# Kernel tuning notes

Measured on AMD Instinct MI355X. Metric: run time of the kernel, lower is better.

The kernel has to match this reference:

```python
import jax, jax.numpy as jnp
import numpy as np

NUM_HEADS = 32
HEAD_DIM = 128
HEAVY_BUDGET = 256
RECENT_BUDGET = 256
ROPE_BASE = 10000.0


def _rope_tables(position_ids, head_dim, dtype):
    inv_freq = 1.0 / (ROPE_BASE ** (jnp.arange(0, head_dim, 2, dtype=jnp.float32) / head_dim))
    freqs = position_ids.astype(jnp.float32)[..., None] * inv_freq  # [b, s, hd/2]
    emb = jnp.concatenate([freqs, freqs], axis=-1)                  # [b, s, hd]
    return jnp.cos(emb).astype(dtype), jnp.sin(emb).astype(dtype)


def _rotate_half(x):
    h = x.shape[-1] // 2
    return jnp.concatenate([-x[..., h:], x[..., :h]], axis=-1)


def setup_inputs() -> dict:
    key = jax.random.key(0)
    k1, k2, k3, k4, k5 = jax.random.split(key, 5)
    b, s, d = 1, 2048, 4096
    hidden_states = jax.random.normal(k1, (b, s, d), dtype=jnp.float32)
    # additive causal mask, as HF passes into forward
    neg = jnp.finfo(jnp.float32).min
    causal = jnp.tril(jnp.ones((s, s), dtype=bool))
    attention_mask = jnp.where(causal, 0.0, neg).astype(jnp.float32)[None, None]  # [1,1,s,s]
    position_ids = jnp.arange(s, dtype=jnp.int32)[None]  # [1, s]
    scale = 0.02
    Wq = jax.random.normal(k2, (d, d), dtype=jnp.float32) * scale
    Wk = jax.random.normal(k3, (d, d), dtype=jnp.float32) * scale
    Wv = jax.random.normal(k4, (d, d), dtype=jnp.float32) * scale
    Wo = jax.random.normal(k5, (d, d), dtype=jnp.float32) * scale
    return {"hidden_states": hidden_states, "attention_mask": attention_mask,
            "position_ids": position_ids, "Wq": Wq, "Wk": Wk, "Wv": Wv, "Wo": Wo}


def reference(hidden_states, attention_mask, position_ids, Wq, Wk, Wv, Wo):
    b, s, d = hidden_states.shape
    H, hd = NUM_HEADS, HEAD_DIM
    kv = s  # prefill: no past_key_value, masks reset

    # projections: nn.Linear(x) = x @ W.T
    q = (hidden_states @ Wq.T).reshape(b, s, H, hd).transpose(0, 2, 1, 3)  # [b,H,s,hd]
    k = (hidden_states @ Wk.T).reshape(b, s, H, hd).transpose(0, 2, 1, 3)
    v = (hidden_states @ Wv.T).reshape(b, s, H, hd).transpose(0, 2, 1, 3)

    cos, sin = _rope_tables(position_ids, hd, q.dtype)  # [b,s,hd]
    cos, sin = cos[:, None], sin[:, None]               # broadcast over heads
    q = q * cos + _rotate_half(q) * sin
    k = k * cos + _rotate_half(k) * sin

    attn = jnp.einsum('bhqd,bhkd->bhqk', q, k) / np.float32(np.sqrt(hd))
    neg = jnp.finfo(attn.dtype).min
    attn = jnp.maximum(attn + attention_mask, neg)
    # attention_masks_next is None on the first (prefill) call -> no multiplicative mask here
    attn = jax.nn.softmax(attn.astype(jnp.float32), axis=-1).astype(q.dtype)  # [b,H,s,kv]

    # running per-head score accumulation: sum over batch and query dims
    scores = attn.sum(axis=0).sum(axis=1)  # [H, kv]; previous_scores is None at prefill

    # heavy-hitter eviction mask for the next decode step (kv+1 columns)
    mask = jnp.ones((H, kv + 1), dtype=attn.dtype)
    # attn_tokens_all (=kv) > cache_budget, recent_budget > 0:
    mask = mask.at[:, :kv + 1 - RECENT_BUDGET].set(0.0)
    selected = scores[:, :kv - RECENT_BUDGET]                    # drop recent region
    _, keep_topk = jax.lax.top_k(selected, HEAVY_BUDGET)         # [H, heavy]
    mask = mask.at[jnp.arange(H)[:, None], keep_topk].set(1.0)   # scatter heavy hitters
    # torch aliasing: score_mask = attn_mask[:, :-1]; score_mask[:, -recent:] = 1 mutates attn_mask too
    mask = mask.at[:, kv - RECENT_BUDGET:kv].set(1.0)
    attention_masks_next = mask[None, :, None, :]                # [1,H,1,kv+1]
    previous_scores = scores * mask[:, :kv]                      # masked score state

    out = jnp.einsum('bhqk,bhkd->bhqd', attn, v)                 # [b,H,s,hd]
    out = out.transpose(0, 2, 1, 3).reshape(b, s, d) @ Wo.T
    return out, attention_masks_next, previous_scores
```

## Files before the change

### kernel.cpp

```cpp
#include <hip/hip_runtime.h>
#include <hip/hip_bf16.h>
#include <cmath>

#define S_LEN 2048
#define DMODEL 4096
#define NH 32
#define HDIM 128
#define HEAVY 256
#define RECENT 256
#define ATTN_SCALE 0.08838834764831845f
#define NEGBIG -3.0e38f
#define MB (1024ull * 1024ull)

typedef __attribute__((ext_vector_type(8))) short short8v;
typedef __attribute__((ext_vector_type(4))) short short4v;
typedef __attribute__((ext_vector_type(4))) float floatx4;

__device__ inline ushort f2bf(float x) {
  __hip_bfloat16 h = __float2bfloat16(x);
  return __builtin_bit_cast(ushort, h);
}
__device__ inline float bf2f(ushort u) {
  __hip_bfloat16 h = __builtin_bit_cast(__hip_bfloat16, u);
  return __bfloat162float(h);
}
struct Split3 {
  short a, b, c;
};
__device__ inline Split3 split3(float x) {
  Split3 o;
  ushort u1 = f2bf(x);
  float r1 = x - bf2f(u1);
  ushort u2 = f2bf(r1);
  float r2 = r1 - bf2f(u2);
  ushort u3 = f2bf(r2);
  o.a = (short)u1;
  o.b = (short)u2;
  o.c = (short)u3;
  return o;
}

__global__ __launch_bounds__(256) void gemm6(const float* __restrict__ A,
                                             const float* __restrict__ B,
                                             float* __restrict__ C, int M, int N, int K) {
  __shared__ short Aa[128 * 40], Ab[128 * 40], Ac[128 * 40];
  __shared__ short Ba[128 * 40], Bb[128 * 40], Bc[128 * 40];
  const int tid = threadIdx.x;
  const int w = tid >> 6, l = tid & 63, g = l >> 4, ln = l & 15;
  const int wm = w >> 1, wn = w & 1;
  const int row0 = blockIdx.y * 128, col0 = blockIdx.x * 128;
  floatx4 acc[4][4] = {};
  for (int k0 = 0; k0 < K; k0 += 32) {
    __syncthreads();
#pragma unroll
    for (int i = 0; i < 4; i++) {
      int id = tid + i * 256;
      int r = id >> 3, c4 = id & 7;
      float4 av = *reinterpret_cast<const float4*>(&A[(size_t)(row0 + r) * K + k0 + c4 * 4]);
      float4 bv = *reinterpret_cast<const float4*>(&B[(size_t)(col0 + r) * K + k0 + c4 * 4]);
      float af[4] = {av.x, av.y, av.z, av.w};
      float bf[4] = {bv.x, bv.y, bv.z, bv.w};
      short4v a1, a2, a3, b1, b2, b3;
#pragma unroll
      for (int j = 0; j < 4; j++) {
        Split3 sa = split3(af[j]);
        Split3 sb = split3(bf[j]);
        a1[j] = sa.a; a2[j] = sa.b; a3[j] = sa.c;
        b1[j] = sb.a; b2[j] = sb.b; b3[j] = sb.c;
      }
      int o = r * 40 + c4 * 4;
      *reinterpret_cast<short4v*>(&Aa[o]) = a1;
      *reinterpret_cast<short4v*>(&Ab[o]) = a2;
      *reinterpret_cast<short4v*>(&Ac[o]) = a3;
      *reinterpret_cast<short4v*>(&Ba[o]) = b1;
      *reinterpret_cast<short4v*>(&Bb[o]) = b2;
      *reinterpret_cast<short4v*>(&Bc[o]) = b3;
    }
    __syncthreads();
#pragma unroll
    for (int i = 0; i < 4; i++) {
      int ar = (wm * 64 + i * 16 + ln) * 40 + g * 8;
      short8v a1 = *reinterpret_cast<const short8v*>(&Aa[ar]);
      short8v a2 = *reinterpret_cast<const short8v*>(&Ab[ar]);
      short8v a3 = *reinterpret_cast<const short8v*>(&Ac[ar]);
#pragma unroll
      for (int j = 0; j < 4; j++) {
        int br = (wn * 64 + j * 16 + ln) * 40 + g * 8;
        short8v b1 = *reinterpret_cast<const short8v*>(&Ba[br]);
        short8v b2 = *reinterpret_cast<const short8v*>(&Bb[br]);
        short8v b3 = *reinterpret_cast<const short8v*>(&Bc[br]);
        acc[i][j] = __builtin_amdgcn_mfma_f32_16x16x32_bf16(a1, b1, acc[i][j], 0, 0, 0);
        acc[i][j] = __builtin_amdgcn_mfma_f32_16x16x32_bf16(a1, b2, acc[i][j], 0, 0, 0);
        acc[i][j] = __builtin_amdgcn_mfma_f32_16x16x32_bf16(a2, b1, acc[i][j], 0, 0, 0);
        acc[i][j] = __builtin_amdgcn_mfma_f32_16x16x32_bf16(a1, b3, acc[i][j], 0, 0, 0);
        acc[i][j] = __builtin_amdgcn_mfma_f32_16x16x32_bf16(a2, b2, acc[i][j], 0, 0, 0);
        acc[i][j] = __builtin_amdgcn_mfma_f32_16x16x32_bf16(a3, b1, acc[i][j], 0, 0, 0);
      }
    }
  }
#pragma unroll
  for (int i = 0; i < 4; i++)
#pragma unroll
    for (int j = 0; j < 4; j++)
#pragma unroll
      for (int r = 0; r < 4; r++)
        C[(size_t)(row0 + wm * 64 + i * 16 + g * 4 + r) * N + col0 + wn * 64 + j * 16 + ln] =
            acc[i][j][r];
}

__global__ __launch_bounds__(256) void gemm_bf1(const float* __restrict__ A,
                                                const float* __restrict__ B,
                                                float* __restrict__ C, int M, int N, int K) {
  __shared__ short Ah[128 * 40];
  __shared__ short Bh[128 * 40];
  const int tid = threadIdx.x;
  const int w = tid >> 6, l = tid & 63, g = l >> 4, ln = l & 15;
  const int wm = w >> 1, wn = w & 1;
  const int row0 = blockIdx.y * 128, col0 = blockIdx.x * 128;
  floatx4 acc[4][4] = {};
  for (int k0 = 0; k0 < K; k0 += 32) {
    __syncthreads();
#pragma unroll
    for (int i = 0; i < 4; i++) {
      int id = tid + i * 256;
      int r = id >> 3, c4 = id & 7;
      float4 av = *reinterpret_cast<const float4*>(&A[(size_t)(row0 + r) * K + k0 + c4 * 4]);
      float4 bv = *reinterpret_cast<const float4*>(&B[(size_t)(col0 + r) * K + k0 + c4 * 4]);
      short4v ah, bh;
      ah[0] = (short)f2bf(av.x); ah[1] = (short)f2bf(av.y);
      ah[2] = (short)f2bf(av.z); ah[3] = (short)f2bf(av.w);
      bh[0] = (short)f2bf(bv.x); bh[1] = (short)f2bf(bv.y);
      bh[2] = (short)f2bf(bv.z); bh[3] = (short)f2bf(bv.w);
      *reinterpret_cast<short4v*>(&Ah[r * 40 + c4 * 4]) = ah;
      *reinterpret_cast<short4v*>(&Bh[r * 40 + c4 * 4]) = bh;
    }
    __syncthreads();
#pragma unroll
    for (int i = 0; i < 4; i++) {
      short8v a = *reinterpret_cast<const short8v*>(&Ah[(wm * 64 + i * 16 + ln) * 40 + g * 8]);
#pragma unroll
      for (int j = 0; j < 4; j++) {
        short8v b = *reinterpret_cast<const short8v*>(&Bh[(wn * 64 + j * 16 + ln) * 40 + g * 8]);
        acc[i][j] = __builtin_amdgcn_mfma_f32_16x16x32_bf16(a, b, acc[i][j], 0, 0, 0);
      }
    }
  }
#pragma unroll
  for (int i = 0; i < 4; i++)
#pragma unroll
    for (int j = 0; j < 4; j++)
#pragma unroll
      for (int r = 0; r < 4; r++)
        C[(size_t)(row0 + wm * 64 + i * 16 + g * 4 + r) * N + col0 + wn * 64 + j * 16 + ln] =
            acc[i][j][r];
}

__global__ __launch_bounds__(256) void gemm_vbt(const float* __restrict__ A,
                                                const float* __restrict__ B,
                                                ushort* __restrict__ Vt, int M, int N, int K) {
  __shared__ short Ah[128 * 40];
  __shared__ short Bh[128 * 40];
  const int tid = threadIdx.x;
  const int w = tid >> 6, l = tid & 63, g = l >> 4, ln = l & 15;
  const int wm = w >> 1, wn = w & 1;
  const int row0 = blockIdx.y * 128, col0 = blockIdx.x * 128;
  floatx4 acc[4][4] = {};
  for (int k0 = 0; k0 < K; k0 += 32) {
    __syncthreads();
#pragma unroll
    for (int i = 0; i < 4; i++) {
      int id = tid + i * 256;
      int r = id >> 3, c4 = id & 7;
      float4 av = *reinterpret_cast<const float4*>(&A[(size_t)(row0 + r) * K + k0 + c4 * 4]);
      float4 bv = *reinterpret_cast<const float4*>(&B[(size_t)(col0 + r) * K + k0 + c4 * 4]);
      short4v ah, bh;
      ah[0] = (short)f2bf(av.x); ah[1] = (short)f2bf(av.y);
      ah[2] = (short)f2bf(av.z); ah[3] = (short)f2bf(av.w);
      bh[0] = (short)f2bf(bv.x); bh[1] = (short)f2bf(bv.y);
      bh[2] = (short)f2bf(bv.z); bh[3] = (short)f2bf(bv.w);
      *reinterpret_cast<short4v*>(&Ah[r * 40 + c4 * 4]) = ah;
      *reinterpret_cast<short4v*>(&Bh[r * 40 + c4 * 4]) = bh;
    }
    __syncthreads();
#pragma unroll
    for (int i = 0; i < 4; i++) {
      short8v a = *reinterpret_cast<const short8v*>(&Ah[(wm * 64 + i * 16 + ln) * 40 + g * 8]);
#pragma unroll
      for (int j = 0; j < 4; j++) {
        short8v b = *reinterpret_cast<const short8v*>(&Bh[(wn * 64 + j * 16 + ln) * 40 + g * 8]);
        acc[i][j] = __builtin_amdgcn_mfma_f32_16x16x32_bf16(a, b, acc[i][j], 0, 0, 0);
      }
    }
  }
#pragma unroll
  for (int i = 0; i < 4; i++)
#pragma unroll
    for (int j = 0; j < 4; j++) {
      short4v o;
#pragma unroll
      for (int r = 0; r < 4; r++) o[r] = (short)f2bf(acc[i][j][r]);
      size_t n = col0 + wn * 64 + j * 16 + ln;
      size_t m0 = row0 + wm * 64 + i * 16 + g * 4;
      *reinterpret_cast<short4v*>(&Vt[n * M + m0]) = o;
    }
}

__global__ void rope_convert(const float* __restrict__ Q, const float* __restrict__ K,
                             const int* __restrict__ pos, short* __restrict__ Qa,
                             short* __restrict__ Qb, short* __restrict__ Qc,
                             short* __restrict__ Ka, short* __restrict__ Kb,
                             short* __restrict__ Kc) {
  int idx = blockIdx.x * blockDim.x + threadIdx.x;
  if (idx >= S_LEN * 64) return;
  int d = idx & 63;
  int r = idx >> 6;
  float p = (float)pos[r];
  float invf = (float)pow(10000.0, -(double)(2 * d) / 128.0);
  float ang = p * invf;
  float c = cosf(ang), s = sinf(ang);
  for (int h = 0; h < NH; h++) {
    size_t base = (size_t)r * DMODEL + h * HDIM + d;
    float q1 = Q[base], q2 = Q[base + 64];
    float k1 = K[base], k2 = K[base + 64];
    float qa = q1 * c - q2 * s, qb = q2 * c + q1 * s;
    float ka = k1 * c - k2 * s, kb = k2 * c + k1 * s;
    Split3 t;
    t = split3(qa); Qa[base] = t.a; Qb[base] = t.b; Qc[base] = t.c;
    t = split3(qb); Qa[base + 64] = t.a; Qb[base + 64] = t.b; Qc[base + 64] = t.c;
    t = split3(ka); Ka[base] = t.a; Kb[base] = t.b; Kc[base] = t.c;
    t = split3(kb); Ka[base + 64] = t.a; Kb[base + 64] = t.b; Kc[base + 64] = t.c;
  }
}

#define KVB 32
#define KTILE_SH (KVB * 128)

__device__ __forceinline__ floatx4 qk6_tile(const short* KaS, const short* KbS,
                                            const short* KcS, const short8v q1[4],
                                            const short8v q2[4], const short8v q3[4],
                                            int krow, int g) {
  floatx4 sacc = {};
#pragma unroll
  for (int dc = 0; dc < 4; dc++) {
    int didx = krow * 128 + ((dc * 32 + g * 8) ^ ((krow & 7) << 3));
    short8v k1 = *reinterpret_cast<const short8v*>(&KaS[didx]);
    short8v k2 = *reinterpret_cast<const short8v*>(&KbS[didx]);
    short8v k3 = *reinterpret_cast<const short8v*>(&KcS[didx]);
    sacc = __builtin_amdgcn_mfma_f32_16x16x32_bf16(q1[dc], k1, sacc, 0, 0, 0);
    sacc = __builtin_amdgcn_mfma_f32_16x16x32_bf16(q1[dc], k2, sacc, 0, 0, 0);
    sacc = __builtin_amdgcn_mfma_f32_16x16x32_bf16(q2[dc], k1, sacc, 0, 0, 0);
    sacc = __builtin_amdgcn_mfma_f32_16x16x32_bf16(q1[dc], k3, sacc, 0, 0, 0);
    sacc = __builtin_amdgcn_mfma_f32_16x16x32_bf16(q2[dc], k2, sacc, 0, 0, 0);
    sacc = __builtin_amdgcn_mfma_f32_16x16x32_bf16(q3[dc], k1, sacc, 0, 0, 0);
  }
  return sacc;
}

__device__ __forceinline__ void stage_load(const short* __restrict__ Ka,
                                           const short* __restrict__ Kb,
                                           const short* __restrict__ Kc, int k0, int h, int tid,
                                           short8v sA[2], short8v sB[2], short8v sC[2]) {
#pragma unroll
  for (int i = 0; i < 2; i++) {
    int id = tid + i * 256;
    int r = id >> 4, c = id & 15;
    size_t goff = (size_t)(k0 + r) * DMODEL + h * HDIM + c * 8;
    sA[i] = *reinterpret_cast<const short8v*>(&Ka[goff]);
    sB[i] = *reinterpret_cast<const short8v*>(&Kb[goff]);
    sC[i] = *reinterpret_cast<const short8v*>(&Kc[goff]);
  }
}

__device__ __forceinline__ void stage_store(short* KaS, short* KbS, short* KcS, int tid,
                                            const short8v sA[2], const short8v sB[2],
                                            const short8v sC[2]) {
#pragma unroll
  for (int i = 0; i < 2; i++) {
    int id = tid + i * 256;
    int r = id >> 4, c = id & 15;
    int didx = r * 128 + ((c * 8) ^ ((r & 7) << 3));
    *reinterpret_cast<short8v*>(&KaS[didx]) = sA[i];
    *reinterpret_cast<short8v*>(&KbS[didx]) = sB[i];
    *reinterpret_cast<short8v*>(&KcS[didx]) = sC[i];
  }
}

__device__ void process_qblock(int qb, int h, const short* __restrict__ Qa,
                               const short* __restrict__ Qb, const short* __restrict__ Qc,
                               const short* __restrict__ Ka, const short* __restrict__ Kb,
                               const short* __restrict__ Kc, const ushort* __restrict__ Vt,
                               float* __restrict__ AO, float* __restrict__ sp4, short* KS0,
                               short* Ps, int tid, int w, int g, int ln) {
  const int q0 = qb * 64;
  const int qrow = q0 + w * 16 + ln;
  short8v q1[4], q2[4], q3[4];
#pragma unroll
  for (int dc = 0; dc < 4; dc++) {
    size_t off = (size_t)qrow * DMODEL + h * HDIM + dc * 32 + g * 8;
    q1[dc] = *reinterpret_cast<const short8v*>(&Qa[off]);
    q2[dc] = *reinterpret_cast<const short8v*>(&Qb[off]);
    q3[dc] = *reinterpret_cast<const short8v*>(&Qc[off]);
  }
  float m_r[4], l_r[4];
#pragma unroll
  for (int r = 0; r < 4; r++) { m_r[r] = NEGBIG; l_r[r] = 0.f; }
  const int nkt = 2 * qb + 2;
  short8v sA[2], sB[2], sC[2];

  stage_load(Ka, Kb, Kc, 0, h, tid, sA, sB, sC);
  stage_store(KS0 + 0, KS0 + KTILE_SH, KS0 + 2 * KTILE_SH, tid, sA, sB, sC);
  __syncthreads();
  for (int t = 0; t < nkt; t++) {
    const int k0 = t * KVB;
    const int cur = t & 1, nxt = cur ^ 1;
    const bool pre = (t + 1 < nkt);
    if (pre) stage_load(Ka, Kb, Kc, k0 + KVB, h, tid, sA, sB, sC);
    short* KaS = KS0 + cur * 3 * KTILE_SH;
    float sv[2][4];
#pragma unroll
    for (int ct = 0; ct < 2; ct++) {
      floatx4 sacc = qk6_tile(KaS, KaS + KTILE_SH, KaS + 2 * KTILE_SH, q1, q2, q3, ct * 16 + ln, g);
#pragma unroll
      for (int r = 0; r < 4; r++) {
        float s = sacc[r] * ATTN_SCALE;
        int key = k0 + ct * 16 + ln;
        int qq = q0 + w * 16 + g * 4 + r;
        sv[ct][r] = (key <= qq) ? s : NEGBIG;
      }
    }
#pragma unroll
    for (int r = 0; r < 4; r++) {
      float tmax = fmaxf(sv[0][r], sv[1][r]);
      tmax = fmaxf(tmax, __shfl_xor(tmax, 1));
      tmax = fmaxf(tmax, __shfl_xor(tmax, 2));
      tmax = fmaxf(tmax, __shfl_xor(tmax, 4));
      tmax = fmaxf(tmax, __shfl_xor(tmax, 8));
      float mnew = fmaxf(m_r[r], tmax);
      float ssum = __expf(sv[0][r] - mnew) + __expf(sv[1][r] - mnew);
      ssum += __shfl_xor(ssum, 1);
      ssum += __shfl_xor(ssum, 2);
      ssum += __shfl_xor(ssum, 4);
      ssum += __shfl_xor(ssum, 8);
      l_r[r] = l_r[r] * __expf(m_r[r] - mnew) + ssum;
      m_r[r] = mnew;
    }
    if (pre) {
      short* KaN = KS0 + nxt * 3 * KTILE_SH;
      stage_store(KaN, KaN + KTILE_SH, KaN + 2 * KTILE_SH, tid, sA, sB, sC);
    }
    __syncthreads();
  }
  float inv_l[4];
#pragma unroll
  for (int r = 0; r < 4; r++) inv_l[r] = 1.0f / l_r[r];

  floatx4 o[8] = {};
  stage_load(Ka, Kb, Kc, 0, h, tid, sA, sB, sC);
  stage_store(KS0 + 0, KS0 + KTILE_SH, KS0 + 2 * KTILE_SH, tid, sA, sB, sC);
  __syncthreads();
  for (int t = 0; t < nkt; t++) {
    const int k0 = t * KVB;
    const int cur = t & 1, nxt = cur ^ 1;
    const bool pre = (t + 1 < nkt);
    if (pre) stage_load(Ka, Kb, Kc, k0 + KVB, h, tid, sA, sB, sC);
    short* KaS = KS0 + cur * 3 * KTILE_SH;
    float pv[2][4];
#pragma unroll
    for (int ct = 0; ct < 2; ct++) {
      floatx4 sacc = qk6_tile(KaS, KaS + KTILE_SH, KaS + 2 * KTILE_SH, q1, q2, q3, ct * 16 + ln, g);
#pragma unroll
      for (int r = 0; r < 4; r++) {
        float s = sacc[r] * ATTN_SCALE;
        int key = k0 + ct * 16 + ln;
        int qq = q0 + w * 16 + g * 4 + r;
        s = (key <= qq) ? s : NEGBIG;
        pv[ct][r] = __expf(s - m_r[r]) * inv_l[r];
      }
    }
#pragma unroll
    for (int ct = 0; ct < 2; ct++) {
      float c2 = pv[ct][0] + pv[ct][1] + pv[ct][2] + pv[ct][3];
      c2 += __shfl_xor(c2, 16);
      c2 += __shfl_xor(c2, 32);
      if (g == 0) sp4[((size_t)(qb * 4 + w) * NH + h) * S_LEN + k0 + ct * 16 + ln] = c2;
    }
#pragma unroll
    for (int ct = 0; ct < 2; ct++)
#pragma unroll
      for (int r = 0; r < 4; r++) {
        int prow = g * 4 + r, pcol = ct * 16 + ln;
        Ps[w * 512 + prow * 32 + (pcol ^ (((prow >> 1) & 1) << 4))] = (short)f2bf(pv[ct][r]);
      }
    short8v pa = *reinterpret_cast<const short8v*>(
        &Ps[w * 512 + ln * 32 + ((g * 8) ^ (((ln >> 1) & 1) << 4))]);
#pragma unroll
    for (int ctd = 0; ctd < 8; ctd++) {
      size_t voff = ((size_t)h * HDIM + ctd * 16 + ln) * S_LEN + k0 + g * 8;
      short8v vb = *reinterpret_cast<const short8v*>(&Vt[voff]);
      o[ctd] = __builtin_amdgcn_mfma_f32_16x16x32_bf16(pa, vb, o[ctd], 0, 0, 0);
    }
    if (pre) {
      short* KaN = KS0 + nxt * 3 * KTILE_SH;
      stage_store(KaN, KaN + KTILE_SH, KaN + 2 * KTILE_SH, tid, sA, sB, sC);
    }
    __syncthreads();
  }
#pragma unroll
  for (int ctd = 0; ctd < 8; ctd++)
#pragma unroll
    for (int r = 0; r < 4; r++)
      AO[(size_t)(q0 + w * 16 + g * 4 + r) * DMODEL + h * HDIM + ctd * 16 + ln] = o[ctd][r];
}

__global__ __launch_bounds__(256) void attn_fused(
    const short* __restrict__ Qa, const short* __restrict__ Qb, const short* __restrict__ Qc,
    const short* __restrict__ Ka, const short* __restrict__ Kb, const short* __restrict__ Kc,
    const ushort* __restrict__ Vt, float* __restrict__ AO, float* __restrict__ sp4) {
  __shared__ short KS[2 * 3 * KTILE_SH];
  __shared__ short Ps[4 * 512];
  const int bid = blockIdx.x;
  const int pid = bid >> 5, h = bid & 31;
  const int tid = threadIdx.x;
  const int w = tid >> 6, l = tid & 63, g = l >> 4, ln = l & 15;
  (void)l;
  process_qblock(31 - pid, h, Qa, Qb, Qc, Ka, Kb, Kc, Vt, AO, sp4, KS, Ps, tid, w, g, ln);
  process_qblock(pid, h, Qa, Qb, Qc, Ka, Kb, Kc, Vt, AO, sp4, KS, Ps, tid, w, g, ln);
}

__global__ void reduce_scores(const float* __restrict__ sp4, float* __restrict__ scores) {
  int idx = blockIdx.x * blockDim.x + threadIdx.x;
  if (idx >= NH * S_LEN) return;
  int h = idx >> 11, k = idx & 2047;
  float s = 0.f;
  for (int j = 0; j < 128; j++) s += sp4[((size_t)j * NH + h) * S_LEN + k];
  scores[idx] = s;
}

__global__ __launch_bounds__(256) void topk_mask_kernel(const float* __restrict__ scores,
                                                        float* __restrict__ out_mask,
                                                        float* __restrict__ prev_scores) {
  const int h = blockIdx.x;
  __shared__ unsigned sb[S_LEN - RECENT];
  __shared__ int cnt_sh;
  const int NSEL = S_LEN - RECENT;
  const int tid = threadIdx.x;
  const float* sc = scores + (size_t)h * S_LEN;
  for (int i = tid; i < NSEL; i += 256) sb[i] = __float_as_uint(sc[i]);
  __syncthreads();
  unsigned prefix = 0u;
  for (int b = 31; b >= 0; b--) {
    unsigned cand = prefix | (1u << b);
    if (tid == 0) cnt_sh = 0;
    __syncthreads();
    int c = 0;
    for (int i = tid; i < NSEL; i += 256) c += (sb[i] >= cand) ? 1 : 0;
    atomicAdd(&cnt_sh, c);
    __syncthreads();
    if (cnt_sh >= HEAVY) prefix = cand;
    __syncthreads();
  }
  if (tid == 0) cnt_sh = 0;
  __syncthreads();
  int c = 0;
  for (int i = tid; i < NSEL; i += 256) c += (sb[i] > prefix) ? 1 : 0;
  atomicAdd(&cnt_sh, c);
  __syncthreads();
  const int c1 = cnt_sh;
  float* mrow = out_mask + (size_t)h * (S_LEN + 1);
  float* prow = prev_scores + (size_t)h * S_LEN;
  for (int j = NSEL + tid; j < S_LEN + 1; j += 256) mrow[j] = 1.0f;
  for (int k = NSEL + tid; k < S_LEN; k += 256) prow[k] = sc[k];
  for (int i = tid; i < NSEL; i += 256) {
    bool sel = sb[i] > prefix;
    mrow[i] = sel ? 1.f : 0.f;
    prow[i] = sel ? sc[i] : 0.f;
  }
  __syncthreads();
  if (tid == 0) {
    int need = HEAVY - c1;
    for (int i = 0; i < NSEL && need > 0; i++) {
      if (sb[i] == prefix) { mrow[i] = 1.f; prow[i] = sc[i]; need--; }
    }
  }
}

extern "C" void kernel_launch(void* const* d_in, const int* in_sizes, int n_in,
                              void* d_out, int out_size, void* d_ws, size_t ws_size,
                              hipStream_t stream) {
  const float* hidden = (const float*)d_in[0];
  const int* pos = (const int*)d_in[2];
  const float* Wq = (const float*)d_in[3];
  const float* Wk = (const float*)d_in[4];
  const float* Wv = (const float*)d_in[5];
  const float* Wo = (const float*)d_in[6];

  float* out0 = (float*)d_out;
  float* out_mask = out0 + (size_t)S_LEN * DMODEL;
  float* prev_scores = out_mask + (size_t)NH * (S_LEN + 1);

  char* ws = (char*)d_ws;
  float* Qf = (float*)(ws + 0 * MB);
  float* Kf = (float*)(ws + 32 * MB);
  ushort* Vt = (ushort*)(ws + 64 * MB);
  short* Qa = (short*)(ws + 80 * MB);
  short* Qb = (short*)(ws + 96 * MB);
  short* Qc = (short*)(ws + 112 * MB);
  short* Ka = (short*)(ws + 128 * MB);
  short* Kb = (short*)(ws + 144 * MB);
  short* Kc = (short*)(ws + 160 * MB);
  float* AO = Qf;
  float* sp4 = Kf;
  float* scores = (float*)(ws + 64 * MB);

  dim3 gg(DMODEL / 128, S_LEN / 128);
  gemm6<<<gg, 256, 0, stream>>>(hidden, Wq, Qf, S_LEN, DMODEL, DMODEL);
  gemm6<<<gg, 256, 0, stream>>>(hidden, Wk, Kf, S_LEN, DMODEL, DMODEL);
  gemm_vbt<<<gg, 256, 0, stream>>>(hidden, Wv, Vt, S_LEN, DMODEL, DMODEL);

  int rope_total = S_LEN * 64;
  rope_convert<<<(rope_total + 255) / 256, 256, 0, stream>>>(Qf, Kf, pos, Qa, Qb, Qc, Ka, Kb, Kc);

  hipError_t _e = hipMemsetAsync(sp4, 0, (size_t)128 * NH * S_LEN * sizeof(float), stream);
  (void)_e;
  attn_fused<<<512, 256, 0, stream>>>(Qa, Qb, Qc, Ka, Kb, Kc, Vt, AO, sp4);

  reduce_scores<<<(NH * S_LEN + 255) / 256, 256, 0, stream>>>(sp4, scores);
  topk_mask_kernel<<<NH, 256, 0, stream>>>(scores, out_mask, prev_scores);

  gemm_bf1<<<gg, 256, 0, stream>>>(AO, Wo, out0, S_LEN, DMODEL, DMODEL);
}
```

Measured before the change: 1.763 ms.

## Pre-split hidden states, use direct global-to-LDS loads in attention, one q-block per CTA

Adds a split_mat pre-pass that splits hidden states once into three bf16 parts, reused by the Q, K and V GEMMs so they no longer resplit the A operand inside the inner loop. split3 now splits by truncating with bit masks instead of round-to-nearest conversions, which changes the numerics slightly. Attention K tiles are staged with global_load_lds so the data skips registers, the six MFMA products go into independent accumulators to break the dependency chain, and the kernel runs one q-block per CTA over a 1024-block grid with an occupancy hint of 3, dropping the paired causal load balancing. The Ha/Hb/Hc buffers share the Qa/Qb/Qc workspace region, which is safe only because rope_convert overwrites them after the GEMMs finish.

Measured after the change: 1.594 ms. -9.6%, faster.

```diff
diff --git a/kernel.cpp b/kernel.cpp
--- a/kernel.cpp
+++ b/kernel.cpp
@@ -20,29 +20,51 @@
   __hip_bfloat16 h = __float2bfloat16(x);
   return __builtin_bit_cast(ushort, h);
 }
-__device__ inline float bf2f(ushort u) {
-  __hip_bfloat16 h = __builtin_bit_cast(__hip_bfloat16, u);
-  return __bfloat162float(h);
-}
 struct Split3 {
   short a, b, c;
 };
 __device__ inline Split3 split3(float x) {
+  unsigned u = __float_as_uint(x);
+  unsigned u1 = u & 0xFFFF0000u;
+  float r1 = x - __uint_as_float(u1);
+  unsigned u2 = __float_as_uint(r1) & 0xFFFF0000u;
+  float r2 = r1 - __uint_as_float(u2);
+  unsigned u3 = __float_as_uint(r2);
   Split3 o;
-  ushort u1 = f2bf(x);
-  float r1 = x - bf2f(u1);
-  ushort u2 = f2bf(r1);
-  float r2 = r1 - bf2f(u2);
-  ushort u3 = f2bf(r2);
-  o.a = (short)u1;
-  o.b = (short)u2;
-  o.c = (short)u3;
+  o.a = (short)(u1 >> 16);
+  o.b = (short)(u2 >> 16);
+  o.c = (short)(u3 >> 16);
   return o;
 }
 
-__global__ __launch_bounds__(256) void gemm6(const float* __restrict__ A,
-                                             const float* __restrict__ B,
-                                             float* __restrict__ C, int M, int N, int K) {
+__device__ __forceinline__ void gl_lds16(const short* gsrc, short* ldst) {
+  __builtin_amdgcn_global_load_lds((const __attribute__((address_space(1))) void*)gsrc,
+                                   (__attribute__((address_space(3))) void*)ldst, 16, 0, 0);
+}
+
+__global__ void split_mat(const float* __restrict__ X, short* __restrict__ Xa,
+                          short* __restrict__ Xb, short* __restrict__ Xc, int n4) {
+  int stride = gridDim.x * blockDim.x;
+  for (int i = blockIdx.x * blockDim.x + threadIdx.x; i < n4; i += stride) {
+    float4 v = reinterpret_cast<const float4*>(X)[i];
+    float vv[4] = {v.x, v.y, v.z, v.w};
+    short4v a, b, c;
+#pragma unroll
+    for (int j = 0; j < 4; j++) {
+      Split3 t = split3(vv[j]);
+      a[j] = t.a; b[j] = t.b; c[j] = t.c;
+    }
+    reinterpret_cast<short4v*>(Xa)[i] = a;
+    reinterpret_cast<short4v*>(Xb)[i] = b;
+    reinterpret_cast<short4v*>(Xc)[i] = c;
+  }
+}
+
+__global__ __launch_bounds__(256) void gemm6h(const short* __restrict__ Aag,
+                                              const short* __restrict__ Abg,
+                                              const short* __restrict__ Acg,
+                                              const float* __restrict__ B,
+                                              float* __restrict__ C, int M, int N, int K) {
   __shared__ short Aa[128 * 40], Ab[128 * 40], Ac[128 * 40];
   __shared__ short Ba[128 * 40], Bb[128 * 40], Bc[128 * 40];
   const int tid = threadIdx.x;
@@ -53,25 +75,28 @@
   for (int k0 = 0; k0 < K; k0 += 32) {
     __syncthreads();
 #pragma unroll
+    for (int i = 0; i < 2; i++) {
+      int id = tid + i * 256;
+      int r = id >> 2, c = id & 3;
+      size_t ga = (size_t)(row0 + r) * K + k0 + c * 8;
+      int o = r * 40 + c * 8;
+      *reinterpret_cast<short8v*>(&Aa[o]) = *reinterpret_cast<const short8v*>(&Aag[ga]);
+      *reinterpret_cast<short8v*>(&Ab[o]) = *reinterpret_cast<const short8v*>(&Abg[ga]);
+      *reinterpret_cast<short8v*>(&Ac[o]) = *reinterpret_cast<const short8v*>(&Acg[ga]);
+    }
+#pragma unroll
     for (int i = 0; i < 4; i++) {
       int id = tid + i * 256;
       int r = id >> 3, c4 = id & 7;
-      float4 av = *reinterpret_cast<const float4*>(&A[(size_t)(row0 + r) * K + k0 + c4 * 4]);
       float4 bv = *reinterpret_cast<const float4*>(&B[(size_t)(col0 + r) * K + k0 + c4 * 4]);
-      float af[4] = {av.x, av.y, av.z, av.w};
       float bf[4] = {bv.x, bv.y, bv.z, bv.w};
-      short4v a1, a2, a3, b1, b2, b3;
+      short4v b1, b2, b3;
 #pragma unroll
       for (int j = 0; j < 4; j++) {
-        Split3 sa = split3(af[j]);
-        Split3 sb = split3(bf[j]);
-        a1[j] = sa.a; a2[j] = sa.b; a3[j] = sa.c;
-        b1[j] = sb.a; b2[j] = sb.b; b3[j] = sb.c;
+        Split3 t = split3(bf[j]);
+        b1[j] = t.a; b2[j] = t.b; b3[j] = t.c;
       }
       int o = r * 40 + c4 * 4;
-      *reinterpret_cast<short4v*>(&Aa[o]) = a1;
-      *reinterpret_cast<short4v*>(&Ab[o]) = a2;
-      *reinterpret_cast<short4v*>(&Ac[o]) = a3;
       *reinterpret_cast<short4v*>(&Ba[o]) = b1;
       *reinterpret_cast<short4v*>(&Bb[o]) = b2;
       *reinterpret_cast<short4v*>(&Bc[o]) = b3;
@@ -155,7 +180,7 @@
             acc[i][j][r];
 }
 
-__global__ __launch_bounds__(256) void gemm_vbt(const float* __restrict__ A,
+__global__ __launch_bounds__(256) void gemm_vbt(const short* __restrict__ Ab2,
                                                 const float* __restrict__ B,
                                                 ushort* __restrict__ Vt, int M, int N, int K) {
   __shared__ short Ah[128 * 40];
@@ -168,17 +193,20 @@
   for (int k0 = 0; k0 < K; k0 += 32) {
     __syncthreads();
 #pragma unroll
+    for (int i = 0; i < 2; i++) {
+      int id = tid + i * 256;
+      int r = id >> 2, c = id & 3;
+      *reinterpret_cast<short8v*>(&Ah[r * 40 + c * 8]) =
+          *reinterpret_cast<const short8v*>(&Ab2[(size_t)(row0 + r) * K + k0 + c * 8]);
+    }
+#pragma unroll
     for (int i = 0; i < 4; i++) {
       int id = tid + i * 256;
       int r = id >> 3, c4 = id & 7;
-      float4 av = *reinterpret_cast<const float4*>(&A[(size_t)(row0 + r) * K + k0 + c4 * 4]);
       float4 bv = *reinterpret_cast<const float4*>(&B[(size_t)(col0 + r) * K + k0 + c4 * 4]);
-      short4v ah, bh;
-      ah[0] = (short)f2bf(av.x); ah[1] = (short)f2bf(av.y);
-      ah[2] = (short)f2bf(av.z); ah[3] = (short)f2bf(av.w);
+      short4v bh;
       bh[0] = (short)f2bf(bv.x); bh[1] = (short)f2bf(bv.y);
       bh[2] = (short)f2bf(bv.z); bh[3] = (short)f2bf(bv.w);
-      *reinterpret_cast<short4v*>(&Ah[r * 40 + c4 * 4]) = ah;
       *reinterpret_cast<short4v*>(&Bh[r * 40 + c4 * 4]) = bh;
     }
     __syncthreads();
@@ -233,64 +261,58 @@
 }
 
 #define KVB 32
-#define KTILE_SH (KVB * 128)
+#define KSPL (KVB * 128)
 
 __device__ __forceinline__ floatx4 qk6_tile(const short* KaS, const short* KbS,
                                             const short* KcS, const short8v q1[4],
                                             const short8v q2[4], const short8v q3[4],
                                             int krow, int g) {
-  floatx4 sacc = {};
+  floatx4 cA = {}, cB = {}, cC = {}, cD = {}, cE = {}, cF = {};
 #pragma unroll
   for (int dc = 0; dc < 4; dc++) {
     int didx = krow * 128 + ((dc * 32 + g * 8) ^ ((krow & 7) << 3));
     short8v k1 = *reinterpret_cast<const short8v*>(&KaS[didx]);
     short8v k2 = *reinterpret_cast<const short8v*>(&KbS[didx]);
     short8v k3 = *reinterpret_cast<const short8v*>(&KcS[didx]);
-    sacc = __builtin_amdgcn_mfma_f32_16x16x32_bf16(q1[dc], k1, sacc, 0, 0, 0);
-    sacc = __builtin_amdgcn_mfma_f32_16x16x32_bf16(q1[dc], k2, sacc, 0, 0, 0);
-    sacc = __builtin_amdgcn_mfma_f32_16x16x32_bf16(q2[dc], k1, sacc, 0, 0, 0);
-    sacc = __builtin_amdgcn_mfma_f32_16x16x32_bf16(q1[dc], k3, sacc, 0, 0, 0);
-    sacc = __builtin_amdgcn_mfma_f32_16x16x32_bf16(q2[dc], k2, sacc, 0, 0, 0);
-    sacc = __builtin_amdgcn_mfma_f32_16x16x32_bf16(q3[dc], k1, sacc, 0, 0, 0);
-  }
-  return sacc;
-}
-
-__device__ __forceinline__ void stage_load(const short* __restrict__ Ka,
+    cA = __builtin_amdgcn_mfma_f32_16x16x32_bf16(q1[dc], k1, cA, 0, 0, 0);
+    cB = __builtin_amdgcn_mfma_f32_16x16x32_bf16(q1[dc], k2, cB, 0, 0, 0);
+    cC = __builtin_amdgcn_mfma_f32_16x16x32_bf16(q2[dc], k1, cC, 0, 0, 0);
+    cD = __builtin_amdgcn_mfma_f32_16x16x32_bf16(q1[dc], k3, cD, 0, 0, 0);
+    cE = __builtin_amdgcn_mfma_f32_16x16x32_bf16(q2[dc], k2, cE, 0, 0, 0);
+    cF = __builtin_amdgcn_mfma_f32_16x16x32_bf16(q3[dc], k1, cF, 0, 0, 0);
+  }
+  return ((cA + cB) + (cC + cD)) + (cE + cF);
+}
+
+__device__ __forceinline__ void issue_tile(const short* __restrict__ Ka,
                                            const short* __restrict__ Kb,
-                                           const short* __restrict__ Kc, int k0, int h, int tid,
-                                           short8v sA[2], short8v sB[2], short8v sC[2]) {
-#pragma unroll
-  for (int i = 0; i < 2; i++) {
-    int id = tid + i * 256;
-    int r = id >> 4, c = id & 15;
-    size_t goff = (size_t)(k0 + r) * DMODEL + h * HDIM + c * 8;
-    sA[i] = *reinterpret_cast<const short8v*>(&Ka[goff]);
-    sB[i] = *reinterpret_cast<const short8v*>(&Kb[goff]);
-    sC[i] = *reinterpret_cast<const short8v*>(&Kc[goff]);
-  }
-}
-
-__device__ __forceinline__ void stage_store(short* KaS, short* KbS, short* KcS, int tid,
-                                            const short8v sA[2], const short8v sB[2],
-                                            const short8v sC[2]) {
-#pragma unroll
-  for (int i = 0; i < 2; i++) {
-    int id = tid + i * 256;
-    int r = id >> 4, c = id & 15;
-    int didx = r * 128 + ((c * 8) ^ ((r & 7) << 3));
-    *reinterpret_cast<short8v*>(&KaS[didx]) = sA[i];
-    *reinterpret_cast<short8v*>(&KbS[didx]) = sB[i];
-    *reinterpret_cast<short8v*>(&KcS[didx]) = sC[i];
-  }
-}
-
-__device__ void process_qblock(int qb, int h, const short* __restrict__ Qa,
-                               const short* __restrict__ Qb, const short* __restrict__ Qc,
-                               const short* __restrict__ Ka, const short* __restrict__ Kb,
-                               const short* __restrict__ Kc, const ushort* __restrict__ Vt,
-                               float* __restrict__ AO, float* __restrict__ sp4, short* KS0,
-                               short* Ps, int tid, int w, int g, int ln) {
+                                           const short* __restrict__ Kc, int k0, int h,
+                                           short* bufA, short* bufB, short* bufC, int tid) {
+  const int wb = tid & 192;
+#pragma unroll
+  for (int it = 0; it < 2; it++) {
+    int j = it * 256 + tid;
+    int r = j >> 4, cl = j & 15;
+    int cg = cl ^ (r & 7);
+    size_t goff = (size_t)(k0 + r) * DMODEL + h * HDIM + cg * 8;
+    int cb = (it * 256 + wb) * 8;
+    gl_lds16(Ka + goff, bufA + cb);
+    gl_lds16(Kb + goff, bufB + cb);
+    gl_lds16(Kc + goff, bufC + cb);
+  }
+}
+
+__global__ __launch_bounds__(256, 3) void attn_fused(
+    const short* __restrict__ Qa, const short* __restrict__ Qb, const short* __restrict__ Qc,
+    const short* __restrict__ Ka, const short* __restrict__ Kb, const short* __restrict__ Kc,
+    const ushort* __restrict__ Vt, float* __restrict__ AO, float* __restrict__ sp4) {
+  __shared__ short KS[2][3][KSPL];
+  __shared__ short Ps[4 * 512];
+  const int bid = blockIdx.x;
+  const int qb = 31 - (bid >> 5);
+  const int h = bid & 31;
+  const int tid = threadIdx.x;
+  const int w = tid >> 6, g = (tid >> 4) & 3, ln = tid & 15;
   const int q0 = qb * 64;
   const int qrow = q0 + w * 16 + ln;
   short8v q1[4], q2[4], q3[4];
@@ -305,21 +327,18 @@
 #pragma unroll
   for (int r = 0; r < 4; r++) { m_r[r] = NEGBIG; l_r[r] = 0.f; }
   const int nkt = 2 * qb + 2;
-  short8v sA[2], sB[2], sC[2];
-
-  stage_load(Ka, Kb, Kc, 0, h, tid, sA, sB, sC);
-  stage_store(KS0 + 0, KS0 + KTILE_SH, KS0 + 2 * KTILE_SH, tid, sA, sB, sC);
+
+  issue_tile(Ka, Kb, Kc, 0, h, KS[0][0], KS[0][1], KS[0][2], tid);
   __syncthreads();
   for (int t = 0; t < nkt; t++) {
     const int k0 = t * KVB;
-    const int cur = t & 1, nxt = cur ^ 1;
-    const bool pre = (t + 1 < nkt);
-    if (pre) stage_load(Ka, Kb, Kc, k0 + KVB, h, tid, sA, sB, sC);
-    short* KaS = KS0 + cur * 3 * KTILE_SH;
+    const int cur = t & 1;
+    if (t + 1 < nkt)
+      issue_tile(Ka, Kb, Kc, k0 + KVB, h, KS[cur ^ 1][0], KS[cur ^ 1][1], KS[cur ^ 1][2], tid);
     float sv[2][4];
 #pragma unroll
     for (int ct = 0; ct < 2; ct++) {
-      floatx4 sacc = qk6_tile(KaS, KaS + KTILE_SH, KaS + 2 * KTILE_SH, q1, q2, q3, ct * 16 + ln, g);
+      floatx4 sacc = qk6_tile(KS[cur][0], KS[cur][1], KS[cur][2], q1, q2, q3, ct * 16 + ln, g);
 #pragma unroll
       for (int r = 0; r < 4; r++) {
         float s = sacc[r] * ATTN_SCALE;
@@ -344,10 +363,6 @@
       l_r[r] = l_r[r] * __expf(m_r[r] - mnew) + ssum;
       m_r[r] = mnew;
     }
-    if (pre) {
-      short* KaN = KS0 + nxt * 3 * KTILE_SH;
-      stage_store(KaN, KaN + KTILE_SH, KaN + 2 * KTILE_SH, tid, sA, sB, sC);
-    }
     __syncthreads();
   }
   float inv_l[4];
@@ -355,19 +370,17 @@
   for (int r = 0; r < 4; r++) inv_l[r] = 1.0f / l_r[r];
 
   floatx4 o[8] = {};
-  stage_load(Ka, Kb, Kc, 0, h, tid, sA, sB, sC);
-  stage_store(KS0 + 0, KS0 + KTILE_SH, KS0 + 2 * KTILE_SH, tid, sA, sB, sC);
+  issue_tile(Ka, Kb, Kc, 0, h, KS[0][0], KS[0][1], KS[0][2], tid);
   __syncthreads();
   for (int t = 0; t < nkt; t++) {
     const int k0 = t * KVB;
-    const int cur = t & 1, nxt = cur ^ 1;
-    const bool pre = (t + 1 < nkt);
-    if (pre) stage_load(Ka, Kb, Kc, k0 + KVB, h, tid, sA, sB, sC);
-    short* KaS = KS0 + cur * 3 * KTILE_SH;
+    const int cur = t & 1;
+    if (t + 1 < nkt)
+      issue_tile(Ka, Kb, Kc, k0 + KVB, h, KS[cur ^ 1][0], KS[cur ^ 1][1], KS[cur ^ 1][2], tid);
     float pv[2][4];
 #pragma unroll
     for (int ct = 0; ct < 2; ct++) {
-      floatx4 sacc = qk6_tile(KaS, KaS + KTILE_SH, KaS + 2 * KTILE_SH, q1, q2, q3, ct * 16 + ln, g);
+      floatx4 sacc = qk6_tile(KS[cur][0], KS[cur][1], KS[cur][2], q1, q2, q3, ct * 16 + ln, g);
 #pragma unroll
       for (int r = 0; r < 4; r++) {
         float s = sacc[r] * ATTN_SCALE;
@@ -399,10 +412,6 @@
       short8v vb = *reinterpret_cast<const short8v*>(&Vt[voff]);
       o[ctd] = __builtin_amdgcn_mfma_f32_16x16x32_bf16(pa, vb, o[ctd], 0, 0, 0);
     }
-    if (pre) {
-      short* KaN = KS0 + nxt * 3 * KTILE_SH;
-      stage_store(KaN, KaN + KTILE_SH, KaN + 2 * KTILE_SH, tid, sA, sB, sC);
-    }
     __syncthreads();
   }
 #pragma unroll
@@ -410,21 +419,6 @@
 #pragma unroll
     for (int r = 0; r < 4; r++)
       AO[(size_t)(q0 + w * 16 + g * 4 + r) * DMODEL + h * HDIM + ctd * 16 + ln] = o[ctd][r];
-}
-
-__global__ __launch_bounds__(256) void attn_fused(
-    const short* __restrict__ Qa, const short* __restrict__ Qb, const short* __restrict__ Qc,
-    const short* __restrict__ Ka, const short* __restrict__ Kb, const short* __restrict__ Kc,
-    const ushort* __restrict__ Vt, float* __restrict__ AO, float* __restrict__ sp4) {
-  __shared__ short KS[2 * 3 * KTILE_SH];
-  __shared__ short Ps[4 * 512];
-  const int bid = blockIdx.x;
-  const int pid = bid >> 5, h = bid & 31;
-  const int tid = threadIdx.x;
-  const int w = tid >> 6, l = tid & 63, g = l >> 4, ln = l & 15;
-  (void)l;
-  process_qblock(31 - pid, h, Qa, Qb, Qc, Ka, Kb, Kc, Vt, AO, sp4, KS, Ps, tid, w, g, ln);
-  process_qblock(pid, h, Qa, Qb, Qc, Ka, Kb, Kc, Vt, AO, sp4, KS, Ps, tid, w, g, ln);
 }
 
 __global__ void reduce_scores(const float* __restrict__ sp4, float* __restrict__ scores) {
@@ -502,6 +496,9 @@
   float* Qf = (float*)(ws + 0 * MB);
   float* Kf = (float*)(ws + 32 * MB);
   ushort* Vt = (ushort*)(ws + 64 * MB);
+  short* Ha = (short*)(ws + 80 * MB);
+  short* Hb = (short*)(ws + 96 * MB);
+  short* Hc = (short*)(ws + 112 * MB);
   short* Qa = (short*)(ws + 80 * MB);
   short* Qb = (short*)(ws + 96 * MB);
   short* Qc = (short*)(ws + 112 * MB);
@@ -513,16 +510,17 @@
   float* scores = (float*)(ws + 64 * MB);
 
   dim3 gg(DMODEL / 128, S_LEN / 128);
-  gemm6<<<gg, 256, 0, stream>>>(hidden, Wq, Qf, S_LEN, DMODEL, DMODEL);
-  gemm6<<<gg, 256, 0, stream>>>(hidden, Wk, Kf, S_LEN, DMODEL, DMODEL);
-  gemm_vbt<<<gg, 256, 0, stream>>>(hidden, Wv, Vt, S_LEN, DMODEL, DMODEL);
+  split_mat<<<2048, 256, 0, stream>>>(hidden, Ha, Hb, Hc, S_LEN * DMODEL / 4);
+  gemm6h<<<gg, 256, 0, stream>>>(Ha, Hb, Hc, Wq, Qf, S_LEN, DMODEL, DMODEL);
+  gemm6h<<<gg, 256, 0, stream>>>(Ha, Hb, Hc, Wk, Kf, S_LEN, DMODEL, DMODEL);
+  gemm_vbt<<<gg, 256, 0, stream>>>(Ha, Wv, Vt, S_LEN, DMODEL, DMODEL);
 
   int rope_total = S_LEN * 64;
   rope_convert<<<(rope_total + 255) / 256, 256, 0, stream>>>(Qf, Kf, pos, Qa, Qb, Qc, Ka, Kb, Kc);
 
   hipError_t _e = hipMemsetAsync(sp4, 0, (size_t)128 * NH * S_LEN * sizeof(float), stream);
   (void)_e;
-  attn_fused<<<512, 256, 0, stream>>>(Qa, Qb, Qc, Ka, Kb, Kc, Vt, AO, sp4);
+  attn_fused<<<1024, 256, 0, stream>>>(Qa, Qb, Qc, Ka, Kb, Kc, Vt, AO, sp4);
 
   reduce_scores<<<(NH * S_LEN + 255) / 256, 256, 0, stream>>>(sp4, scores);
   topk_mask_kernel<<<NH, 256, 0, stream>>>(scores, out_mask, prev_scores);
```
